# Optimization experiments

Hardware: AMD Instinct MI355X
Metric: run time of the kernel (lower is better)

Reference implementation:

```python
import jax, jax.numpy as jnp
import numpy as np

U, I, D, E = 100000, 50000, 128, 3200000


def setup_inputs() -> dict:
    key = jax.random.key(0)
    k0, k1, k2, k3, k4 = jax.random.split(key, 5)
    stdv = 1.0 / np.sqrt(D)
    return {
        "user_embedding": jax.random.uniform(k0, (U, D), jnp.float32, -stdv, stdv),
        "item_embedding": jax.random.uniform(k1, (I, D), jnp.float32, -stdv, stdv),
        "edge_vals": jax.random.uniform(k2, (E,), jnp.float32),  # normalized adj values
        "edge_u": jax.random.randint(k3, (E,), 0, U, jnp.int32),
        "edge_i": jax.random.randint(k4, (E,), 0, I, jnp.int32),
        "n_layers": 3,
    }


def reference(user_embedding, item_embedding, edge_vals, edge_u, edge_i, n_layers):
    # LightGCN forward: alternate SpMM on bipartite graph G [U,I] (COO edges),
    # then average embeddings across layers 0..n_layers.
    num_users = user_embedding.shape[0]
    num_items = item_embedding.shape[0]
    u_list = [user_embedding]
    i_list = [item_embedding]
    w = edge_vals[:, None]  # [E,1]
    for layer in range(n_layers):
        # u_{l+1} = G @ i_l : gather item rows along edges, scale, scatter-add to users
        new_u = jax.ops.segment_sum(w * i_list[layer][edge_i], edge_u,
                                    num_segments=num_users)
        # i_{l+1} = G^T @ u_l
        new_i = jax.ops.segment_sum(w * u_list[layer][edge_u], edge_i,
                                    num_segments=num_items)
        u_list.append(new_u)
        i_list.append(new_i)
    denom = jnp.float32(n_layers + 1)
    embed_user = sum(u_list) / denom
    embed_item = sum(i_list) / denom
    return (embed_user, embed_item)
```

## Files before the change

kernel.cpp:

```cpp
#include <hip/hip_runtime.h>


#define D 128
#define CHUNK 16384
#define CTILE 64
#define SRCMASK 0x3FFFF
#define TPB 256
#define RS_CAP 6144

typedef unsigned int u32x2 __attribute__((ext_vector_type(2)));
typedef float f32x4 __attribute__((ext_vector_type(4)));

__device__ inline uint2 ntload_u2(const uint2* p) {
    u32x2 v = __builtin_nontemporal_load((const u32x2*)p);
    uint2 r; r.x = v.x; r.y = v.y; return r;
}
__device__ inline void ntstore_f4(float* p, float4 v) {
    f32x4 t; t.x = v.x; t.y = v.y; t.z = v.z; t.w = v.w;
    __builtin_nontemporal_store(t, (f32x4*)p);
}
__device__ inline int ntload_i(const int* p) { return __builtin_nontemporal_load(p); }
__device__ inline float ntload_f(const float* p) { return __builtin_nontemporal_load(p); }
__device__ inline float4 ntload_f4(const float* p) {
    f32x4 v = __builtin_nontemporal_load((const f32x4*)p);
    return make_float4(v.x, v.y, v.z, v.w);
}

__device__ inline unsigned pack4(float a, float b, float c, float d, float qs) {
    int q0 = __float2int_rn(a * qs), q1 = __float2int_rn(b * qs);
    int q2 = __float2int_rn(c * qs), q3 = __float2int_rn(d * qs);
    return ((unsigned)(q0 & 255)) | ((unsigned)(q1 & 255) << 8) |
           ((unsigned)(q2 & 255) << 16) | ((unsigned)(q3 & 255) << 24);
}

__device__ inline void acc_q8(float4& sa, float4& sb, uint2 raw, float m) {
    unsigned x = raw.x, y = raw.y;
    sa.x += m * (float)((int)(x << 24) >> 24);
    sa.y += m * (float)((int)(x << 16) >> 24);
    sa.z += m * (float)((int)(x <<  8) >> 24);
    sa.w += m * (float)((int)(x      ) >> 24);
    sb.x += m * (float)((int)(y << 24) >> 24);
    sb.y += m * (float)((int)(y << 16) >> 24);
    sb.z += m * (float)((int)(y <<  8) >> 24);
    sb.w += m * (float)((int)(y      ) >> 24);
}

__global__ __launch_bounds__(TPB) void k_quant8(
    const float* __restrict__ ue, const float* __restrict__ ie,
    uint2* __restrict__ h0q, float* __restrict__ sc0, int U, int UA, int NP) {
    int row = blockIdx.x * (TPB / 16) + (threadIdx.x >> 4);
    if (row >= NP) return;
    int lane = threadIdx.x & 15;
    float4 a = make_float4(0.f, 0.f, 0.f, 0.f);
    float4 b = make_float4(0.f, 0.f, 0.f, 0.f);
    const float* p = nullptr;
    if (row < U)        p = ue + (size_t)row * D + lane * 8;
    else if (row >= UA) p = ie + (size_t)(row - UA) * D + lane * 8;
    if (p) { a = ntload_f4(p); b = ntload_f4(p + 4); }
    float m = fmaxf(fmaxf(fmaxf(fabsf(a.x), fabsf(a.y)), fmaxf(fabsf(a.z), fabsf(a.w))),
                    fmaxf(fmaxf(fabsf(b.x), fabsf(b.y)), fmaxf(fabsf(b.z), fabsf(b.w))));
    for (int d_ = 1; d_ < 16; d_ <<= 1) m = fmaxf(m, __shfl_xor(m, d_));
    float qs = (m > 0.f) ? 127.f / m : 0.f;
    uint2 q;
    q.x = pack4(a.x, a.y, a.z, a.w, qs);
    q.y = pack4(b.x, b.y, b.z, b.w, qs);
    h0q[(size_t)row * 16 + lane] = q;
    if (lane == 0) sc0[row] = m * (1.f / 127.f);
}

__global__ __launch_bounds__(256) void k_count(const int* __restrict__ eu,
                                               const int* __restrict__ ei,
                                               int* __restrict__ C, int E, int NB, int UA) {
    extern __shared__ int hist[];
    for (int k = threadIdx.x; k < NB; k += blockDim.x) hist[k] = 0;
    __syncthreads();
    int base = blockIdx.x * CHUNK;
    int n = min(CHUNK, E - base);
    for (int t = threadIdx.x; t < n; t += blockDim.x) {
        int u = ntload_i(eu + base + t);
        int i = ntload_i(ei + base + t);
        atomicAdd(&hist[u >> 6], 1);
        atomicAdd(&hist[(UA + i) >> 6], 1);
    }
    __syncthreads();
    int* Crow = C + (size_t)blockIdx.x * NB;
    for (int k = threadIdx.x; k < NB; k += blockDim.x) Crow[k] = hist[k];
}

__global__ __launch_bounds__(256) void k_tile_sum(const int* __restrict__ C,
                                                  int* __restrict__ S, int NB, int NC) {
    int b = blockIdx.x * 256 + threadIdx.x;
    if (b >= NB) return;
    int tc = blockIdx.y;
    int c0 = tc * CTILE, c1 = min(c0 + CTILE, NC);
    int s = 0;
    for (int c = c0; c < c1; ++c) s += C[(size_t)c * NB + b];
    S[(size_t)tc * NB + b] = s;
}

__global__ __launch_bounds__(256) void k_super(int* __restrict__ S, int* __restrict__ T,
                                               int NB, int TC) {
    int b = blockIdx.x * 256 + threadIdx.x;
    if (b >= NB) return;
    int run = 0;
    for (int tc = 0; tc < TC; ++tc) {
        size_t k = (size_t)tc * NB + b;
        int v = S[k];
        S[k] = run;
        run += v;
    }
    T[b] = run;
}

__global__ __launch_bounds__(1024) void k_scan(const int* __restrict__ T,
                                               int* __restrict__ offb, int N) {
    __shared__ int partial[1024];
    int t = threadIdx.x;
    int CH = (N + 1023) >> 10;
    int c0 = min(t * CH, N), c1 = min(c0 + CH, N);
    int sum = 0;
    for (int k = c0; k < c1; ++k) sum += T[k];
    partial[t] = sum;
    __syncthreads();
    for (int s = 1; s < 1024; s <<= 1) {
        int add = (t >= s) ? partial[t - s] : 0;
        __syncthreads();
        partial[t] += add;
        __syncthreads();
    }
    int run = (t == 0) ? 0 : partial[t - 1];
    for (int k = c0; k < c1; ++k) { offb[k] = run; run += T[k]; }
    if (t == 0) offb[N] = partial[1023];
}

__global__ __launch_bounds__(256) void k_colscan(const int* __restrict__ C,
                                                 const int* __restrict__ S,
                                                 const int* __restrict__ offb,
                                                 int* __restrict__ colScan, int NB, int NC) {
    int b = blockIdx.x * 256 + threadIdx.x;
    if (b >= NB) return;
    int tc = blockIdx.y;
    int c0 = tc * CTILE, c1 = min(c0 + CTILE, NC);
    int run = offb[b] + S[(size_t)tc * NB + b];
    for (int c = c0; c < c1; ++c) {
        size_t k = (size_t)c * NB + b;
        colScan[k] = run;
        run += C[k];
    }
}

__global__ __launch_bounds__(256) void k_cscatter(
    const int* __restrict__ eu, const int* __restrict__ ei, const float* __restrict__ w,
    const int* __restrict__ colScan, uint2* __restrict__ entA, int E, int NB, int UA) {
    extern __shared__ int cursor[];
    int c = blockIdx.x, t = threadIdx.x;
    const int* cs = colScan + (size_t)c * NB;
    for (int k = t; k < NB; k += 256) cursor[k] = cs[k];
    __syncthreads();
    int base = c * CHUNK;
    int n = min(CHUNK, E - base);
    for (int k = t; k < n; k += 256) {
        int u = ntload_i(eu + base + k);
        int gi = UA + ntload_i(ei + base + k);
        unsigned wb = __float_as_uint(ntload_f(w + base + k));
        int pA = atomicAdd(&cursor[u >> 6], 1);
        entA[pA] = make_uint2(((unsigned)(u & 63) << 18) | (unsigned)gi, wb);
        int pB = atomicAdd(&cursor[gi >> 6], 1);
        entA[pB] = make_uint2(((unsigned)(gi & 63) << 18) | (unsigned)u, wb);
    }
}

__global__ __launch_bounds__(256) void k_rowsort(
    const uint2* __restrict__ entA, uint2* __restrict__ entB,
    const int* __restrict__ offb, int* __restrict__ off, int NP) {
    __shared__ int hist[64];
    __shared__ int rowOff[64];
    __shared__ int cursor[64];
    __shared__ uint2 ebuf[RS_CAP];
    int b = blockIdx.x, t = threadIdx.x;
    int segBase = offb[b];
    int len = offb[b + 1] - segBase;
    if (t < 64) hist[t] = 0;
    __syncthreads();
    if (len <= RS_CAP) {
        for (int k = t; k < len; k += 256) {
            uint2 e = ntload_u2(entA + segBase + k);
            ebuf[k] = e;
            atomicAdd(&hist[e.x >> 18], 1);
        }
        __syncthreads();
        if (t == 0) {
            int run = 0;
            for (int r = 0; r < 64; ++r) { rowOff[r] = run; cursor[r] = run; run += hist[r]; }
        }
        __syncthreads();
        for (int k = t; k < len; k += 256) {
            uint2 e = ebuf[k];
            int p = atomicAdd(&cursor[e.x >> 18], 1);
            entB[segBase + p] = e;
        }
    } else {
        for (int k = t; k < len; k += 256)
            atomicAdd(&hist[ntload_u2(entA + segBase + k).x >> 18], 1);
        __syncthreads();
        if (t == 0) {
            int run = 0;
            for (int r = 0; r < 64; ++r) { rowOff[r] = run; cursor[r] = run; run += hist[r]; }
        }
        __syncthreads();
        for (int k = t; k < len; k += 256) {
            uint2 e = ntload_u2(entA + segBase + k);
            int p = atomicAdd(&cursor[e.x >> 18], 1);
            entB[segBase + p] = e;
        }
    }
    __syncthreads();
    if (t < 64) {
        int g = b * 64 + t;
        if (g <= NP) off[g] = segBase + rowOff[t];
    }
}

template <int MODE>
__global__ __launch_bounds__(TPB) void k_spmm(
    const uint2* __restrict__ q, const float* __restrict__ sc,
    uint2* __restrict__ nxtq, float* __restrict__ scn,
    const uint2* __restrict__ e1q, const float* __restrict__ sc1,
    const uint2* __restrict__ e2q, const float* __restrict__ sc2,
    const float* __restrict__ ue, const float* __restrict__ ie,
    float* __restrict__ out,
    const int* __restrict__ off, const uint2* __restrict__ csr,
    int U, int UA, int rowBase, int rowCnt) {
    int row = rowBase + blockIdx.x * (TPB / 16) + (threadIdx.x >> 4);
    if (row >= rowBase + rowCnt) return;
    int lane = threadIdx.x & 15;
    int beg = off[row], end = off[row + 1];
    float4 sa = make_float4(0.f, 0.f, 0.f, 0.f);
    float4 sb = make_float4(0.f, 0.f, 0.f, 0.f);

    int nIter = (end - beg) >> 2;
    int p = beg;
    if (nIter > 0) {
        uint2 m0 = csr[p], m1 = csr[p + 1], m2 = csr[p + 2], m3 = csr[p + 3];
        for (int it = 0; it < nIter; ++it) {
            int s0 = m0.x & SRCMASK, s1 = m1.x & SRCMASK;
            int s2 = m2.x & SRCMASK, s3 = m3.x & SRCMASK;
            uint2 g0 = q[(size_t)s0 * 16 + lane];
            uint2 g1 = q[(size_t)s1 * 16 + lane];
            uint2 g2 = q[(size_t)s2 * 16 + lane];
            uint2 g3 = q[(size_t)s3 * 16 + lane];
            float f0 = __uint_as_float(m0.y) * sc[s0];
            float f1 = __uint_as_float(m1.y) * sc[s1];
            float f2 = __uint_as_float(m2.y) * sc[s2];
            float f3 = __uint_as_float(m3.y) * sc[s3];
            int pn = p + 4;
            if (it + 1 < nIter) {
                m0 = csr[pn];     m1 = csr[pn + 1];
                m2 = csr[pn + 2]; m3 = csr[pn + 3];
            }
            acc_q8(sa, sb, g0, f0);
            acc_q8(sa, sb, g1, f1);
            acc_q8(sa, sb, g2, f2);
            acc_q8(sa, sb, g3, f3);
            p = pn;
        }
    }
    for (; p < end; ++p) {
        uint2 m_ = csr[p];
        int s_ = m_.x & SRCMASK;
        uint2 g_ = q[(size_t)s_ * 16 + lane];
        acc_q8(sa, sb, g_, __uint_as_float(m_.y) * sc[s_]);
    }

    if (MODE == 0) {
        float m = fmaxf(fmaxf(fmaxf(fabsf(sa.x), fabsf(sa.y)), fmaxf(fabsf(sa.z), fabsf(sa.w))),
                        fmaxf(fmaxf(fabsf(sb.x), fabsf(sb.y)), fmaxf(fabsf(sb.z), fabsf(sb.w))));
        for (int d_ = 1; d_ < 16; d_ <<= 1) m = fmaxf(m, __shfl_xor(m, d_));
        float qs = (m > 0.f) ? 127.f / m : 0.f;
        uint2 qo;
        qo.x = pack4(sa.x, sa.y, sa.z, sa.w, qs);
        qo.y = pack4(sb.x, sb.y, sb.z, sb.w, qs);
        nxtq[(size_t)row * 16 + lane] = qo;
        if (lane == 0) scn[row] = m * (1.f / 127.f);
    } else {
        int outRow;
        const float* e0p;
        if (row < U)        { outRow = row;            e0p = ue + (size_t)row * D + lane * 8; }
        else if (row >= UA) { outRow = U + (row - UA); e0p = ie + (size_t)(row - UA) * D + lane * 8; }
        else return;
        float4 e0a = ntload_f4(e0p);
        float4 e0b = ntload_f4(e0p + 4);
        uint2 q1 = e1q[(size_t)row * 16 + lane]; float s1r = sc1[row];
        uint2 q2 = e2q[(size_t)row * 16 + lane]; float s2r = sc2[row];
        unsigned x1 = q1.x, y1 = q1.y, x2 = q2.x, y2 = q2.y;
        float4 ra, rb;
        ra.x = 0.25f * (e0a.x + s1r * (float)((int)(x1 << 24) >> 24) + s2r * (float)((int)(x2 << 24) >> 24) + sa.x);
        ra.y = 0.25f * (e0a.y + s1r * (float)((int)(x1 << 16) >> 24) + s2r * (float)((int)(x2 << 16) >> 24) + sa.y);
        ra.z = 0.25f * (e0a.z + s1r * (float)((int)(x1 <<  8) >> 24) + s2r * (float)((int)(x2 <<  8) >> 24) + sa.z);
        ra.w = 0.25f * (e0a.w + s1r * (float)((int)(x1      ) >> 24) + s2r * (float)((int)(x2      ) >> 24) + sa.w);
        rb.x = 0.25f * (e0b.x + s1r * (float)((int)(y1 << 24) >> 24) + s2r * (float)((int)(y2 << 24) >> 24) + sb.x);
        rb.y = 0.25f * (e0b.y + s1r * (float)((int)(y1 << 16) >> 24) + s2r * (float)((int)(y2 << 16) >> 24) + sb.y);
        rb.z = 0.25f * (e0b.z + s1r * (float)((int)(y1 <<  8) >> 24) + s2r * (float)((int)(y2 <<  8) >> 24) + sb.z);
        rb.w = 0.25f * (e0b.w + s1r * (float)((int)(y1      ) >> 24) + s2r * (float)((int)(y2      ) >> 24) + sb.w);
        float* op = out + (size_t)outRow * D + lane * 8;
        ntstore_f4(op, ra);
        ntstore_f4(op + 4, rb);
    }
}

extern "C" void kernel_launch(void* const* d_in, const int* in_sizes, int n_in,
                              void* d_out, int out_size, void* d_ws, size_t ws_size,
                              hipStream_t stream) {
    const float* ue = (const float*)d_in[0];
    const float* ie = (const float*)d_in[1];
    const float* w  = (const float*)d_in[2];
    const int*   eu = (const int*)d_in[3];
    const int*   ei = (const int*)d_in[4];

    const int U  = in_sizes[0] / D;
    const int I  = in_sizes[1] / D;
    const int E  = in_sizes[2];
    const int UA = ((U + 63) >> 6) << 6;
    const int NP = UA + I;
    const int NB = (NP + 63) >> 6;
    const int NC = (E + CHUNK - 1) / CHUNK;
    const int TC = (NC + CTILE - 1) / CTILE;
    const size_t nE2 = (size_t)2 * E;

    uint2* h0q = (uint2*)d_ws;
    uint2* e1q = h0q + (size_t)NP * 16;
    uint2* e2q = e1q + (size_t)NP * 16;
    float* sc0 = (float*)(e2q + (size_t)NP * 16);
    float* sc1 = sc0 + NP;
    float* sc2 = sc1 + NP;
    uint2* entB = (uint2*)(sc2 + NP);
    int* C       = (int*)(entB + nE2);
    int* colScan = C + (size_t)NC * NB;
    int* S       = colScan + (size_t)NC * NB;
    int* T       = S + (size_t)TC * NB;
    int* offb    = T + NB;
    int* off     = offb + NB + 1;
    char* tail   = (char*)(off + NP + 1);
    tail += (8 - ((uintptr_t)tail & 7)) & 7;
    uint2* entA  = (uint2*)tail;

    const size_t needed = (size_t)NP * D * 3 + (size_t)NP * 12
                        + nE2 * 8 * 2
                        + ((size_t)2 * NC * NB + (size_t)TC * NB + NB + (NB + 1) + (NP + 1)) * 4 + 8;
    if (ws_size < needed) return;

    const int nbR = (NP + 15) / 16;
    const int nbU = (UA + 15) / 16;
    const int nbI = (I + 15) / 16;
    const int TB = (NB + 255) / 256;

    k_quant8<<<nbR, TPB, 0, stream>>>(ue, ie, h0q, sc0, U, UA, NP);
    k_count<<<NC, 256, (size_t)NB * 4, stream>>>(eu, ei, C, E, NB, UA);
    k_tile_sum<<<dim3(TB, TC), 256, 0, stream>>>(C, S, NB, NC);
    k_super<<<TB, 256, 0, stream>>>(S, T, NB, TC);
    k_scan<<<1, 1024, 0, stream>>>(T, offb, NB);
    k_colscan<<<dim3(TB, TC), 256, 0, stream>>>(C, S, offb, colScan, NB, NC);
    k_cscatter<<<NC, 256, (size_t)NB * 4, stream>>>(eu, ei, w, colScan, entA, E, NB, UA);
    k_rowsort<<<NB, 256, 0, stream>>>(entA, entB, offb, off, NP);

    k_spmm<0><<<nbU, TPB, 0, stream>>>(h0q, sc0, e1q, sc1, nullptr, nullptr, nullptr, nullptr,
                                       ue, ie, nullptr, off, entB, U, UA, 0, UA);
    k_spmm<0><<<nbI, TPB, 0, stream>>>(h0q, sc0, e1q, sc1, nullptr, nullptr, nullptr, nullptr,
                                       ue, ie, nullptr, off, entB, U, UA, UA, I);
    k_spmm<0><<<nbU, TPB, 0, stream>>>(e1q, sc1, e2q, sc2, nullptr, nullptr, nullptr, nullptr,
                                       ue, ie, nullptr, off, entB, U, UA, 0, UA);
    k_spmm<0><<<nbI, TPB, 0, stream>>>(e1q, sc1, e2q, sc2, nullptr, nullptr, nullptr, nullptr,
                                       ue, ie, nullptr, off, entB, U, UA, UA, I);
    k_spmm<1><<<nbU, TPB, 0, stream>>>(e2q, sc2, nullptr, nullptr, e1q, sc1, e2q, sc2,
                                       ue, ie, (float*)d_out, off, entB, U, UA, 0, UA);
    k_spmm<1><<<nbI, TPB, 0, stream>>>(e2q, sc2, nullptr, nullptr, e1q, sc1, e2q, sc2,
                                       ue, ie, (float*)d_out, off, entB, U, UA, UA, I);
}
```

Measured before the change: 644.3 us.

## Replace single-pass edge scatter with two-level superbucket radix partition

Edge bucketing now runs in two levels. k_split partitions each chunk's edges into 4096-row superbuckets. k_sbscatter then distributes each superbucket into 64-row buckets using the per-chunk column scan offsets. The aim is better write locality, since scattering directly into roughly 2300 fine buckets gives poorly coalesced random writes. In exchange it adds an extra full read and write of the doubled edge list, a larger workspace, and a halved CHUNK size that doubles the count-matrix size.

```diff
diff --git a/kernel.cpp b/kernel.cpp
--- a/kernel.cpp
+++ b/kernel.cpp
@@ -2,11 +2,13 @@
 
 
 #define D 128
-#define CHUNK 16384
+#define CHUNK 8192
 #define CTILE 64
 #define SRCMASK 0x3FFFF
 #define TPB 256
 #define RS_CAP 6144
+#define NSPLIT 16
+#define SPLIT_GRID 128
 
 typedef unsigned int u32x2 __attribute__((ext_vector_type(2)));
 typedef float f32x4 __attribute__((ext_vector_type(4)));
@@ -70,7 +72,8 @@
 
 __global__ __launch_bounds__(256) void k_count(const int* __restrict__ eu,
                                                const int* __restrict__ ei,
-                                               int* __restrict__ C, int E, int NB, int UA) {
+                                               int* __restrict__ C, int* __restrict__ C2,
+                                               int E, int NB, int NS, int UA) {
     extern __shared__ int hist[];
     for (int k = threadIdx.x; k < NB; k += blockDim.x) hist[k] = 0;
     __syncthreads();
@@ -85,6 +88,13 @@
     __syncthreads();
     int* Crow = C + (size_t)blockIdx.x * NB;
     for (int k = threadIdx.x; k < NB; k += blockDim.x) Crow[k] = hist[k];
+    int* C2row = C2 + (size_t)blockIdx.x * NS;
+    for (int s = threadIdx.x; s < NS; s += blockDim.x) {
+        int b0 = s * 64, b1 = min(b0 + 64, NB);
+        int acc = 0;
+        for (int b = b0; b < b1; ++b) acc += hist[b];
+        C2row[s] = acc;
+    }
 }
 
 __global__ __launch_bounds__(256) void k_tile_sum(const int* __restrict__ C,
@@ -149,24 +159,65 @@
     }
 }
 
-__global__ __launch_bounds__(256) void k_cscatter(
+__global__ __launch_bounds__(256) void k_split(
     const int* __restrict__ eu, const int* __restrict__ ei, const float* __restrict__ w,
-    const int* __restrict__ colScan, uint2* __restrict__ entA, int E, int NB, int UA) {
-    extern __shared__ int cursor[];
-    int c = blockIdx.x, t = threadIdx.x;
-    const int* cs = colScan + (size_t)c * NB;
-    for (int k = t; k < NB; k += 256) cursor[k] = cs[k];
-    __syncthreads();
-    int base = c * CHUNK;
-    int n = min(CHUNK, E - base);
-    for (int k = t; k < n; k += 256) {
-        int u = ntload_i(eu + base + k);
-        int gi = UA + ntload_i(ei + base + k);
-        unsigned wb = __float_as_uint(ntload_f(w + base + k));
-        int pA = atomicAdd(&cursor[u >> 6], 1);
-        entA[pA] = make_uint2(((unsigned)(u & 63) << 18) | (unsigned)gi, wb);
-        int pB = atomicAdd(&cursor[gi >> 6], 1);
-        entA[pB] = make_uint2(((unsigned)(gi & 63) << 18) | (unsigned)u, wb);
+    const int* __restrict__ C2, int* __restrict__ P2, uint2* __restrict__ sbA,
+    int E, int NC, int NS, int UA) {
+    __shared__ int cur[64];
+    __shared__ int tmp[64];
+    int t = threadIdx.x;
+    for (int c = blockIdx.x; c < NC; c += gridDim.x) {
+        if (t < NS) tmp[t] = C2[(size_t)c * NS + t];
+        __syncthreads();
+        if (t == 0) {
+            int run = c * 2 * CHUNK;
+            for (int s = 0; s < NS; ++s) {
+                int v = tmp[s];
+                cur[s] = run;
+                P2[(size_t)c * NS + s] = run;
+                run += v;
+            }
+        }
+        __syncthreads();
+        int base = c * CHUNK;
+        int n = min(CHUNK, E - base);
+        for (int k = t; k < n; k += 256) {
+            int u  = ntload_i(eu + base + k);
+            int gi = UA + ntload_i(ei + base + k);
+            unsigned wb = __float_as_uint(ntload_f(w + base + k));
+            int pu = atomicAdd(&cur[u >> 12], 1);
+            sbA[pu] = make_uint2(((unsigned)(u & 4095) << 18) | (unsigned)gi, wb);
+            int pi = atomicAdd(&cur[gi >> 12], 1);
+            sbA[pi] = make_uint2(((unsigned)(gi & 4095) << 18) | (unsigned)u, wb);
+        }
+        __syncthreads();
+    }
+}
+
+__global__ __launch_bounds__(256) void k_sbscatter(
+    const uint2* __restrict__ sbA, uint2* __restrict__ bkt,
+    const int* __restrict__ C2, const int* __restrict__ P2,
+    const int* __restrict__ colScan, int NB, int NC, int NS) {
+    __shared__ int cur[64];
+    int s = blockIdx.y;
+    int j = blockIdx.x;
+    int CL = (NC + NSPLIT - 1) / NSPLIT;
+    int c0 = j * CL, c1 = min(NC, c0 + CL);
+    if (c0 >= c1) return;
+    int t = threadIdx.x;
+    int b0 = s * 64;
+    int nb = min(64, NB - b0);
+    if (t < nb) cur[t] = colScan[(size_t)c0 * NB + b0 + t];
+    __syncthreads();
+    for (int c = c0; c < c1; ++c) {
+        int start = P2[(size_t)c * NS + s];
+        int len   = C2[(size_t)c * NS + s];
+        for (int k = t; k < len; k += 256) {
+            uint2 e = ntload_u2(sbA + start + k);
+            int bl = (int)((e.x >> 24) & 63u);
+            int p = atomicAdd(&cur[bl], 1);
+            bkt[p] = e;
+        }
     }
 }
 
@@ -186,7 +237,7 @@
         for (int k = t; k < len; k += 256) {
             uint2 e = ntload_u2(entA + segBase + k);
             ebuf[k] = e;
-            atomicAdd(&hist[e.x >> 18], 1);
+            atomicAdd(&hist[(e.x >> 18) & 63u], 1);
         }
         __syncthreads();
         if (t == 0) {
@@ -196,12 +247,12 @@
         __syncthreads();
         for (int k = t; k < len; k += 256) {
             uint2 e = ebuf[k];
-            int p = atomicAdd(&cursor[e.x >> 18], 1);
+            int p = atomicAdd(&cursor[(e.x >> 18) & 63u], 1);
             entB[segBase + p] = e;
         }
     } else {
         for (int k = t; k < len; k += 256)
-            atomicAdd(&hist[ntload_u2(entA + segBase + k).x >> 18], 1);
+            atomicAdd(&hist[(ntload_u2(entA + segBase + k).x >> 18) & 63u], 1);
         __syncthreads();
         if (t == 0) {
             int run = 0;
@@ -210,7 +261,7 @@
         __syncthreads();
         for (int k = t; k < len; k += 256) {
             uint2 e = ntload_u2(entA + segBase + k);
-            int p = atomicAdd(&cursor[e.x >> 18], 1);
+            int p = atomicAdd(&cursor[(e.x >> 18) & 63u], 1);
             entB[segBase + p] = e;
         }
     }
@@ -323,9 +374,11 @@
     const int UA = ((U + 63) >> 6) << 6;
     const int NP = UA + I;
     const int NB = (NP + 63) >> 6;
+    const int NS = (NP + 4095) >> 12;
     const int NC = (E + CHUNK - 1) / CHUNK;
     const int TC = (NC + CTILE - 1) / CTILE;
     const size_t nE2 = (size_t)2 * E;
+    const size_t nX  = (size_t)NC * 2 * CHUNK;
 
     uint2* h0q = (uint2*)d_ws;
     uint2* e1q = h0q + (size_t)NP * 16;
@@ -333,20 +386,21 @@
     float* sc0 = (float*)(e2q + (size_t)NP * 16);
     float* sc1 = sc0 + NP;
     float* sc2 = sc1 + NP;
-    uint2* entB = (uint2*)(sc2 + NP);
-    int* C       = (int*)(entB + nE2);
+    uint2* X   = (uint2*)(sc2 + NP);
+    uint2* Y   = X + nX;
+    int* C       = (int*)(Y + nE2);
     int* colScan = C + (size_t)NC * NB;
     int* S       = colScan + (size_t)NC * NB;
     int* T       = S + (size_t)TC * NB;
     int* offb    = T + NB;
     int* off     = offb + NB + 1;
-    char* tail   = (char*)(off + NP + 1);
-    tail += (8 - ((uintptr_t)tail & 7)) & 7;
-    uint2* entA  = (uint2*)tail;
+    int* C2      = off + NP + 1;
+    int* P2      = C2 + (size_t)NC * NS;
 
     const size_t needed = (size_t)NP * D * 3 + (size_t)NP * 12
-                        + nE2 * 8 * 2
-                        + ((size_t)2 * NC * NB + (size_t)TC * NB + NB + (NB + 1) + (NP + 1)) * 4 + 8;
+                        + (nX + nE2) * 8
+                        + ((size_t)2 * NC * NB + (size_t)TC * NB + NB + (NB + 1)
+                           + (NP + 1) + (size_t)2 * NC * NS) * 4;
     if (ws_size < needed) return;
 
     const int nbR = (NP + 15) / 16;
@@ -355,24 +409,25 @@
     const int TB = (NB + 255) / 256;
 
     k_quant8<<<nbR, TPB, 0, stream>>>(ue, ie, h0q, sc0, U, UA, NP);
-    k_count<<<NC, 256, (size_t)NB * 4, stream>>>(eu, ei, C, E, NB, UA);
+    k_count<<<NC, 256, (size_t)NB * 4, stream>>>(eu, ei, C, C2, E, NB, NS, UA);
     k_tile_sum<<<dim3(TB, TC), 256, 0, stream>>>(C, S, NB, NC);
     k_super<<<TB, 256, 0, stream>>>(S, T, NB, TC);
     k_scan<<<1, 1024, 0, stream>>>(T, offb, NB);
     k_colscan<<<dim3(TB, TC), 256, 0, stream>>>(C, S, offb, colScan, NB, NC);
-    k_cscatter<<<NC, 256, (size_t)NB * 4, stream>>>(eu, ei, w, colScan, entA, E, NB, UA);
-    k_rowsort<<<NB, 256, 0, stream>>>(entA, entB, offb, off, NP);
+    k_split<<<SPLIT_GRID, 256, 0, stream>>>(eu, ei, w, C2, P2, X, E, NC, NS, UA);
+    k_sbscatter<<<dim3(NSPLIT, NS), 256, 0, stream>>>(X, Y, C2, P2, colScan, NB, NC, NS);
+    k_rowsort<<<NB, 256, 0, stream>>>(Y, X, offb, off, NP);
 
     k_spmm<0><<<nbU, TPB, 0, stream>>>(h0q, sc0, e1q, sc1, nullptr, nullptr, nullptr, nullptr,
-                                       ue, ie, nullptr, off, entB, U, UA, 0, UA);
+                                       ue, ie, nullptr, off, X, U, UA, 0, UA);
     k_spmm<0><<<nbI, TPB, 0, stream>>>(h0q, sc0, e1q, sc1, nullptr, nullptr, nullptr, nullptr,
-                                       ue, ie, nullptr, off, entB, U, UA, UA, I);
+                                       ue, ie, nullptr, off, X, U, UA, UA, I);
     k_spmm<0><<<nbU, TPB, 0, stream>>>(e1q, sc1, e2q, sc2, nullptr, nullptr, nullptr, nullptr,
-                                       ue, ie, nullptr, off, entB, U, UA, 0, UA);
+                                       ue, ie, nullptr, off, X, U, UA, 0, UA);
     k_spmm<0><<<nbI, TPB, 0, stream>>>(e1q, sc1, e2q, sc2, nullptr, nullptr, nullptr, nullptr,
-                                       ue, ie, nullptr, off, entB, U, UA, UA, I);
+                                       ue, ie, nullptr, off, X, U, UA, UA, I);
     k_spmm<1><<<nbU, TPB, 0, stream>>>(e2q, sc2, nullptr, nullptr, e1q, sc1, e2q, sc2,
-                                       ue, ie, (float*)d_out, off, entB, U, UA, 0, UA);
+                                       ue, ie, (float*)d_out, off, X, U, UA, 0, UA);
     k_spmm<1><<<nbI, TPB, 0, stream>>>(e2q, sc2, nullptr, nullptr, e1q, sc1, e2q, sc2,
-                                       ue, ie, (float*)d_out, off, entB, U, UA, UA, I);
-}
+                                       ue, ie, (float*)d_out, off, X, U, UA, UA, I);
+}
```

Result: no change. 635.7 us (-1.3%).
